# Performance work log

Measured on AMD Instinct MI355X. Metric: run time of the kernel, lower is better.

The kernel has to match this reference:

```python
import jax, jax.numpy as jnp
import numpy as np

N = 50000
E = 800000
IN_DIM = 256
HID = 64
HEADS = 4
OUT_DIM = 32
NEG_SLOPE = 0.2
EPS = 1e-5


def segment_softmax(logits, seg, num_segments):
    # logits: [E, H]; softmax over edges sharing the same destination node
    m = jax.ops.segment_max(logits, seg, num_segments=num_segments)
    m = jnp.where(jnp.isfinite(m), m, 0.0)
    e = jnp.exp(logits - m[seg])
    s = jax.ops.segment_sum(e, seg, num_segments=num_segments)
    return e / (s[seg] + 1e-16)


def setup_inputs() -> dict:
    key = jax.random.key(0)
    ks = jax.random.split(key, 16)
    d = {}
    d['x'] = jax.random.normal(ks[0], (N, IN_DIM), dtype=jnp.float32)
    d['edge_index'] = jax.random.randint(ks[1], (2, E), 0, N, dtype=jnp.int64)
    sc = lambda fan: 1.0 / np.sqrt(fan)
    # input transform: Linear(256->128), Linear(128->64)
    d['t1_w'] = jax.random.normal(ks[2], (IN_DIM, IN_DIM // 2), dtype=jnp.float32) * sc(IN_DIM)
    d['t1_b'] = jnp.zeros((IN_DIM // 2,), jnp.float32)
    d['t2_w'] = jax.random.normal(ks[3], (IN_DIM // 2, IN_DIM // 4), dtype=jnp.float32) * sc(IN_DIM // 2)
    d['t2_b'] = jnp.zeros((IN_DIM // 4,), jnp.float32)
    d['g1_w'] = jax.random.normal(ks[4], (IN_DIM // 4, HEADS * HID), dtype=jnp.float32) * sc(IN_DIM // 4)
    d['g1_att_src'] = jax.random.normal(ks[5], (HEADS, HID), dtype=jnp.float32) * sc(HID)
    d['g1_att_dst'] = jax.random.normal(ks[6], (HEADS, HID), dtype=jnp.float32) * sc(HID)
    d['g1_b'] = jnp.zeros((HEADS * HID,), jnp.float32)
    # GraphNorm(256)
    d['gn_w'] = jnp.ones((HEADS * HID,), jnp.float32)
    d['gn_b'] = jnp.zeros((HEADS * HID,), jnp.float32)
    d['gn_ms'] = jnp.ones((HEADS * HID,), jnp.float32)
    # GATConv 2: 256 -> 32, 1 head, no concat (mean == identity for 1 head)
    d['g2_w'] = jax.random.normal(ks[7], (HEADS * HID, OUT_DIM), dtype=jnp.float32) * sc(HEADS * HID)
    d['g2_att_src'] = jax.random.normal(ks[8], (1, OUT_DIM), dtype=jnp.float32) * sc(OUT_DIM)
    d['g2_att_dst'] = jax.random.normal(ks[9], (1, OUT_DIM), dtype=jnp.float32) * sc(OUT_DIM)
    d['g2_b'] = jnp.zeros((OUT_DIM,), jnp.float32)
    return d


def gat_conv(x, src, dst, w, att_src, att_dst, bias, n_nodes):
    heads, ch = att_src.shape
    h = (x @ w).reshape(n_nodes, heads, ch)            # [N,H,C]
    a_src = jnp.sum(h * att_src, axis=-1)              # [N,H]
    a_dst = jnp.sum(h * att_dst, axis=-1)              # [N,H]
    logits = jax.nn.leaky_relu(a_src[src] + a_dst[dst], NEG_SLOPE)  # [E,H]
    alpha = segment_softmax(logits, dst, n_nodes)      # [E,H]
    msgs = alpha[:, :, None] * h[src]                  # [E,H,C]
    out = jax.ops.segment_sum(msgs, dst, num_segments=n_nodes)  # [N,H,C]
    return out.reshape(n_nodes, heads * ch) + bias


def reference(x, edge_index, t1_w, t1_b, t2_w, t2_b,
              g1_w, g1_att_src, g1_att_dst, g1_b,
              gn_w, gn_b, gn_ms,
              g2_w, g2_att_src, g2_att_dst, g2_b):
    src, dst = edge_index[0], edge_index[1]
    # input transform (dropout inactive in eval)
    h = jax.nn.relu(x @ t1_w + t1_b)
    h = jax.nn.relu(h @ t2_w + t2_b)
    # GAT layer 1 (concat heads)
    h = gat_conv(h, src, dst, g1_w, g1_att_src, g1_att_dst, g1_b, N)
    # GraphNorm over the whole graph (batch=None -> single graph)
    mean = jnp.mean(h, axis=0)
    o = h - mean * gn_ms
    var = jnp.mean(o * o, axis=0)
    h = o / jnp.sqrt(var + EPS) * gn_w + gn_b
    h = jax.nn.elu(h)
    # GAT layer 2 (1 head, concat=False)
    h = gat_conv(h, src, dst, g2_w, g2_att_src, g2_att_dst, g2_b, N)
    return jax.nn.log_softmax(h, axis=1)
```

## Files before the change

kernel.cpp:

```cpp
#include <hip/hip_runtime.h>

#define NSLOPE 0.2f
#define GEPS 1e-5f

typedef unsigned short ushortT;
typedef __attribute__((ext_vector_type(8))) unsigned short us8;
typedef __attribute__((ext_vector_type(8))) __bf16 bf16x8;
typedef __attribute__((ext_vector_type(4))) float f32x4;

__device__ __forceinline__ float lrelu(float x) { return x >= 0.f ? x : NSLOPE * x; }
__device__ __forceinline__ ushortT f2bf(float f) {
    unsigned int u = __float_as_uint(f);
    return (ushortT)((u + 0x7fffu + ((u >> 16) & 1u)) >> 16);
}
__device__ __forceinline__ float bf2f(ushortT h) {
    return __uint_as_float((unsigned int)h << 16);
}

__global__ __launch_bounds__(256) void k_prep_hist(
    const float* __restrict__ w1, const float* __restrict__ w2,
    const float* __restrict__ g1w, const float* __restrict__ g2w,
    ushortT* __restrict__ w1t, ushortT* __restrict__ w2t,
    ushortT* __restrict__ g1t, ushortT* __restrict__ g2t,
    const int* __restrict__ dst, int* __restrict__ deg, int E)
{
    if (blockIdx.x >= 128) {
        const int i = (blockIdx.x - 128) * 256 + threadIdx.x;
        if (i < E) atomicAdd(&deg[dst[i]], 1);
        return;
    }
    const int i = blockIdx.x * 256 + threadIdx.x;
    if (i < 128 * 256) { const int c = i >> 8, k = i & 255; w1t[i] = f2bf(w1[k * 128 + c]); }
    if (i < 64 * 128)  { const int c = i >> 7, k = i & 127; w2t[i] = f2bf(w2[k * 64 + c]); }
    if (i < 256 * 64)  { const int c = i >> 6, k = i & 63;  g1t[i] = f2bf(g1w[k * 256 + c]); }
    if (i < 32 * 256)  { const int c = i >> 8, k = i & 255; g2t[i] = f2bf(g2w[k * 32 + c]); }
}

__global__ __launch_bounds__(256) void k_lin1(const float* __restrict__ x,
    const ushortT* __restrict__ w1t, const float* __restrict__ b1,
    ushortT* __restrict__ h1, int n,
    const int* __restrict__ deg, int* __restrict__ offs, int* __restrict__ bsum, int gemmB)
{
    if ((int)blockIdx.x >= gemmB) {
        __shared__ int sm[256];
        const int t = threadIdx.x;
        const int i = (blockIdx.x - gemmB) * 256 + t;
        const int v = (i < n) ? deg[i] : 0;
        sm[t] = v;
        __syncthreads();
        for (int off = 1; off < 256; off <<= 1) {
            int add = (t >= off) ? sm[t - off] : 0;
            __syncthreads();
            sm[t] += add;
            __syncthreads();
        }
        if (i < n) offs[i] = sm[t] - v;
        if (t == 255) bsum[blockIdx.x - gemmB] = sm[255];
        return;
    }
    __shared__ us8 Ab[64 * 128 / 16];
    __shared__ us8 Bb[128 * 128 / 16];
    char* A = (char*)Ab; char* B = (char*)Bb;
    const int t = threadIdx.x;
    const int w = t >> 6, l = t & 63;
    const int lo = l & 15, hi = l >> 4;
    const int n0 = blockIdx.x * 64;
    const int wm = (w >> 1) * 32, wn = (w & 1) * 64;
    f32x4 acc[2][4];
    #pragma unroll
    for (int mf = 0; mf < 2; ++mf)
        #pragma unroll
        for (int nf = 0; nf < 4; ++nf) acc[mf][nf] = (f32x4){0.f, 0.f, 0.f, 0.f};

    const int arow = t >> 2, ak0 = (t & 3) * 16;
    int agn = n0 + arow; if (agn >= n) agn = n - 1;
    const int asw = (arow & 7) << 4;

    for (int kc = 0; kc < 4; ++kc) {
        __syncthreads();
        {
            ushortT tmp[16];
            const float* xp = &x[(size_t)agn * 256 + kc * 64 + ak0];
            #pragma unroll
            for (int j = 0; j < 4; ++j) {
                const float4 v = *(const float4*)(xp + j * 4);
                tmp[j*4+0] = f2bf(v.x); tmp[j*4+1] = f2bf(v.y);
                tmp[j*4+2] = f2bf(v.z); tmp[j*4+3] = f2bf(v.w);
            }
            *(us8*)(A + arow * 128 + ((ak0 * 2) ^ asw)) = *(us8*)tmp;
            *(us8*)(A + arow * 128 + ((ak0 * 2 + 16) ^ asw)) = *(us8*)(tmp + 8);
        }
        #pragma unroll
        for (int i = 0; i < 4; ++i) {
            const int idx = i * 256 + t, br = idx >> 3, bs = idx & 7;
            const us8 v = *(const us8*)&w1t[(size_t)br * 256 + kc * 64 + bs * 8];
            *(us8*)(B + br * 128 + ((bs * 16) ^ ((br & 7) << 4))) = v;
        }
        __syncthreads();
        #pragma unroll
        for (int ks = 0; ks < 2; ++ks) {
            const int koff = ks * 64 + hi * 16;
            bf16x8 af[2], bf[4];
            #pragma unroll
            for (int mf = 0; mf < 2; ++mf) {
                const int r = wm + mf * 16 + lo;
                af[mf] = *(const bf16x8*)(A + r * 128 + (koff ^ ((r & 7) << 4)));
            }
            #pragma unroll
            for (int nf = 0; nf < 4; ++nf) {
                const int r = wn + nf * 16 + lo;
                bf[nf] = *(const bf16x8*)(B + r * 128 + (koff ^ ((r & 7) << 4)));
            }
            #pragma unroll
            for (int mf = 0; mf < 2; ++mf)
                #pragma unroll
                for (int nf = 0; nf < 4; ++nf)
                    acc[mf][nf] = __builtin_amdgcn_mfma_f32_16x16x32_bf16(af[mf], bf[nf], acc[mf][nf], 0, 0, 0);
        }
    }
    #pragma unroll
    for (int nf = 0; nf < 4; ++nf) {
        const int col = wn + nf * 16 + lo;
        const float bb = b1[col];
        #pragma unroll
        for (int mf = 0; mf < 2; ++mf)
            #pragma unroll
            for (int j = 0; j < 4; ++j) {
                const int r = n0 + wm + mf * 16 + hi * 4 + j;
                if (r < n) h1[(size_t)r * 128 + col] = f2bf(fmaxf(acc[mf][nf][j] + bb, 0.f));
            }
    }
}

__global__ __launch_bounds__(256) void k_lin2(const ushortT* __restrict__ h1,
    const ushortT* __restrict__ w2t, const float* __restrict__ b2,
    ushortT* __restrict__ h2, int n,
    int* __restrict__ bsum, int nb, int gemmB)
{
    if ((int)blockIdx.x >= gemmB) {
        __shared__ int sm[256];
        const int t = threadIdx.x;
        const int v = (t < nb) ? bsum[t] : 0;
        sm[t] = v;
        __syncthreads();
        for (int off = 1; off < 256; off <<= 1) {
            int add = (t >= off) ? sm[t - off] : 0;
            __syncthreads();
            sm[t] += add;
            __syncthreads();
        }
        if (t < nb) bsum[t] = sm[t] - v;
        return;
    }
    __shared__ us8 Ab[64 * 128 / 16];
    __shared__ us8 Bb[64 * 128 / 16];
    char* A = (char*)Ab; char* B = (char*)Bb;
    const int t = threadIdx.x;
    const int w = t >> 6, l = t & 63;
    const int lo = l & 15, hi = l >> 4;
    const int n0 = blockIdx.x * 64;
    const int wm = (w >> 1) * 32, wn = (w & 1) * 32;
    f32x4 acc[2][2];
    #pragma unroll
    for (int mf = 0; mf < 2; ++mf)
        #pragma unroll
        for (int nf = 0; nf < 2; ++nf) acc[mf][nf] = (f32x4){0.f, 0.f, 0.f, 0.f};

    const int arow = t >> 2, ak0 = (t & 3) * 16;
    int agn = n0 + arow; if (agn >= n) agn = n - 1;
    const int asw = (arow & 7) << 4;

    for (int kc = 0; kc < 2; ++kc) {
        __syncthreads();
        {
            const us8 v0 = *(const us8*)&h1[(size_t)agn * 128 + kc * 64 + ak0];
            const us8 v1 = *(const us8*)&h1[(size_t)agn * 128 + kc * 64 + ak0 + 8];
            *(us8*)(A + arow * 128 + ((ak0 * 2) ^ asw)) = v0;
            *(us8*)(A + arow * 128 + ((ak0 * 2 + 16) ^ asw)) = v1;
        }
        #pragma unroll
        for (int i = 0; i < 2; ++i) {
            const int idx = i * 256 + t, br = idx >> 3, bs = idx & 7;
            const us8 v = *(const us8*)&w2t[(size_t)br * 128 + kc * 64 + bs * 8];
            *(us8*)(B + br * 128 + ((bs * 16) ^ ((br & 7) << 4))) = v;
        }
        __syncthreads();
        #pragma unroll
        for (int ks = 0; ks < 2; ++ks) {
            const int koff = ks * 64 + hi * 16;
            bf16x8 af[2], bf[2];
            #pragma unroll
            for (int mf = 0; mf < 2; ++mf) {
                const int r = wm + mf * 16 + lo;
                af[mf] = *(const bf16x8*)(A + r * 128 + (koff ^ ((r & 7) << 4)));
            }
            #pragma unroll
            for (int nf = 0; nf < 2; ++nf) {
                const int r = wn + nf * 16 + lo;
                bf[nf] = *(const bf16x8*)(B + r * 128 + (koff ^ ((r & 7) << 4)));
            }
            #pragma unroll
            for (int mf = 0; mf < 2; ++mf)
                #pragma unroll
                for (int nf = 0; nf < 2; ++nf)
                    acc[mf][nf] = __builtin_amdgcn_mfma_f32_16x16x32_bf16(af[mf], bf[nf], acc[mf][nf], 0, 0, 0);
        }
    }
    #pragma unroll
    for (int nf = 0; nf < 2; ++nf) {
        const int col = wn + nf * 16 + lo;
        const float bb = b2[col];
        #pragma unroll
        for (int mf = 0; mf < 2; ++mf)
            #pragma unroll
            for (int j = 0; j < 4; ++j) {
                const int r = n0 + wm + mf * 16 + hi * 4 + j;
                if (r < n) h2[(size_t)r * 64 + col] = f2bf(fmaxf(acc[mf][nf][j] + bb, 0.f));
            }
    }
}

__global__ __launch_bounds__(256) void k_g1feat(const ushortT* __restrict__ h2,
    const ushortT* __restrict__ g1t, const float* __restrict__ attS, const float* __restrict__ attD,
    ushortT* __restrict__ hg1, float* __restrict__ a1s, float* __restrict__ a1d, int n,
    int* __restrict__ offs, int* __restrict__ cursor, const int* __restrict__ bsum, int E, int gemmB)
{
    if ((int)blockIdx.x >= gemmB) {
        const int sb = blockIdx.x - gemmB;
        const int i = sb * 256 + threadIdx.x;
        if (i < n) {
            int o = offs[i] + bsum[i >> 8];
            offs[i] = o;
            cursor[i] = o;
        }
        if (i == 0) offs[n] = E;
        return;
    }
    __shared__ us8 Ab[64 * 128 / 16];
    __shared__ us8 Bb[256 * 128 / 16];
    char* A = (char*)Ab; char* B = (char*)Bb;
    const int t = threadIdx.x;
    const int w = t >> 6, l = t & 63;
    const int lo = l & 15, hi = l >> 4;
    const int n0 = blockIdx.x * 64;
    const int wm = (w >> 1) * 32, wn = (w & 1) * 128;
    f32x4 acc[2][8];
    #pragma unroll
    for (int mf = 0; mf < 2; ++mf)
        #pragma unroll
        for (int nf = 0; nf < 8; ++nf) acc[mf][nf] = (f32x4){0.f, 0.f, 0.f, 0.f};

    {
        const int arow = t >> 2, ak0 = (t & 3) * 16;
        int agn = n0 + arow; if (agn >= n) agn = n - 1;
        const int asw = (arow & 7) << 4;
        const us8 v0 = *(const us8*)&h2[(size_t)agn * 64 + ak0];
        const us8 v1 = *(const us8*)&h2[(size_t)agn * 64 + ak0 + 8];
        *(us8*)(A + arow * 128 + ((ak0 * 2) ^ asw)) = v0;
        *(us8*)(A + arow * 128 + ((ak0 * 2 + 16) ^ asw)) = v1;
    }
    #pragma unroll
    for (int i = 0; i < 8; ++i) {
        const int idx = i * 256 + t, br = idx >> 3, bs = idx & 7;
        const us8 v = *(const us8*)&g1t[(size_t)br * 64 + bs * 8];
        *(us8*)(B + br * 128 + ((bs * 16) ^ ((br & 7) << 4))) = v;
    }
    __syncthreads();
    #pragma unroll
    for (int ks = 0; ks < 2; ++ks) {
        const int koff = ks * 64 + hi * 16;
        bf16x8 af[2];
        #pragma unroll
        for (int mf = 0; mf < 2; ++mf) {
            const int r = wm + mf * 16 + lo;
            af[mf] = *(const bf16x8*)(A + r * 128 + (koff ^ ((r & 7) << 4)));
        }
        #pragma unroll
        for (int nf = 0; nf < 8; ++nf) {
            const int r = wn + nf * 16 + lo;
            const bf16x8 bf = *(const bf16x8*)(B + r * 128 + (koff ^ ((r & 7) << 4)));
            #pragma unroll
            for (int mf = 0; mf < 2; ++mf)
                acc[mf][nf] = __builtin_amdgcn_mfma_f32_16x16x32_bf16(af[mf], bf, acc[mf][nf], 0, 0, 0);
        }
    }
    float sS[8], sD[8];
    #pragma unroll
    for (int nf = 0; nf < 8; ++nf) {
        sS[nf] = attS[wn + nf * 16 + lo];
        sD[nf] = attD[wn + nf * 16 + lo];
    }
    const int hA = wn >> 6, hB = hA + 1;
    #pragma unroll
    for (int mf = 0; mf < 2; ++mf)
        #pragma unroll
        for (int j = 0; j < 4; ++j) {
            const int r = n0 + wm + mf * 16 + hi * 4 + j;
            float pSA = 0.f, pDA = 0.f, pSB = 0.f, pDB = 0.f;
            #pragma unroll
            for (int nf = 0; nf < 4; ++nf) {
                pSA = fmaf(acc[mf][nf][j], sS[nf], pSA);
                pDA = fmaf(acc[mf][nf][j], sD[nf], pDA);
                pSB = fmaf(acc[mf][nf + 4][j], sS[nf + 4], pSB);
                pDB = fmaf(acc[mf][nf + 4][j], sD[nf + 4], pDB);
            }
            #pragma unroll
            for (int off = 1; off < 16; off <<= 1) {
                pSA += __shfl_xor(pSA, off);
                pDA += __shfl_xor(pDA, off);
                pSB += __shfl_xor(pSB, off);
                pDB += __shfl_xor(pDB, off);
            }
            if (r < n) {
                if (lo == 0) {
                    a1s[r * 4 + hA] = pSA; a1s[r * 4 + hB] = pSB;
                    a1d[r * 4 + hA] = pDA; a1d[r * 4 + hB] = pDB;
                }
                #pragma unroll
                for (int nf = 0; nf < 8; ++nf)
                    hg1[(size_t)r * 256 + wn + nf * 16 + lo] = f2bf(acc[mf][nf][j]);
            }
        }
}

__global__ __launch_bounds__(256) void k_g2feat(const ushortT* __restrict__ out1,
    const float* __restrict__ colsum, const float* __restrict__ colsq,
    const float* __restrict__ gw, const float* __restrict__ gb, const float* __restrict__ gms,
    const ushortT* __restrict__ g2t, const float* __restrict__ attS, const float* __restrict__ attD,
    ushortT* __restrict__ hg2, float* __restrict__ a2s, float* __restrict__ a2d, int n)
{
    __shared__ us8 Ab[64 * 128 / 16];
    __shared__ us8 Bb[32 * 128 / 16];
    __shared__ float lsc[256], lsh[256];
    char* A = (char*)Ab; char* B = (char*)Bb;
    const int t = threadIdx.x;
    const int w = t >> 6, l = t & 63;
    const int lo = l & 15, hi = l >> 4;
    const int n0 = blockIdx.x * 64;
    const int wm = w * 16;
    {
        const float invn = 1.f / (float)n;
        const float mean = colsum[t] * invn;
        const float msq = colsq[t] * invn;
        const float ms = gms[t];
        const float var = msq - 2.f * ms * mean * mean + ms * ms * mean * mean;
        const float sc = gw[t] * rsqrtf(var + GEPS);
        lsc[t] = sc;
        lsh[t] = gb[t] - mean * ms * sc;
    }
    f32x4 acc[2];
    acc[0] = (f32x4){0.f, 0.f, 0.f, 0.f};
    acc[1] = (f32x4){0.f, 0.f, 0.f, 0.f};

    const int arow = t >> 2, ak0 = (t & 3) * 16;
    int agn = n0 + arow; if (agn >= n) agn = n - 1;
    const int asw = (arow & 7) << 4;

    for (int kc = 0; kc < 4; ++kc) {
        __syncthreads();
        {
            ushortT tmp[16];
            const us8 v0 = *(const us8*)&out1[(size_t)agn * 256 + kc * 64 + ak0];
            const us8 v1 = *(const us8*)&out1[(size_t)agn * 256 + kc * 64 + ak0 + 8];
            #pragma unroll
            for (int j = 0; j < 8; ++j) {
                float a = bf2f(v0[j]) * lsc[kc * 64 + ak0 + j] + lsh[kc * 64 + ak0 + j];
                float b = bf2f(v1[j]) * lsc[kc * 64 + ak0 + 8 + j] + lsh[kc * 64 + ak0 + 8 + j];
                a = a > 0.f ? a : __expf(a) - 1.f;
                b = b > 0.f ? b : __expf(b) - 1.f;
                tmp[j] = f2bf(a); tmp[8 + j] = f2bf(b);
            }
            *(us8*)(A + arow * 128 + ((ak0 * 2) ^ asw)) = *(us8*)tmp;
            *(us8*)(A + arow * 128 + ((ak0 * 2 + 16) ^ asw)) = *(us8*)(tmp + 8);
        }
        {
            const int br = t >> 3, bs = t & 7;
            const us8 v = *(const us8*)&g2t[(size_t)br * 256 + kc * 64 + bs * 8];
            *(us8*)(B + br * 128 + ((bs * 16) ^ ((br & 7) << 4))) = v;
        }
        __syncthreads();
        #pragma unroll
        for (int ks = 0; ks < 2; ++ks) {
            const int koff = ks * 64 + hi * 16;
            const int ra = wm + lo;
            const bf16x8 af = *(const bf16x8*)(A + ra * 128 + (koff ^ ((ra & 7) << 4)));
            #pragma unroll
            for (int nf = 0; nf < 2; ++nf) {
                const int r = nf * 16 + lo;
                const bf16x8 bf = *(const bf16x8*)(B + r * 128 + (koff ^ ((r & 7) << 4)));
                acc[nf] = __builtin_amdgcn_mfma_f32_16x16x32_bf16(af, bf, acc[nf], 0, 0, 0);
            }
        }
    }
    float sS[2], sD[2];
    sS[0] = attS[lo]; sS[1] = attS[16 + lo];
    sD[0] = attD[lo]; sD[1] = attD[16 + lo];
    #pragma unroll
    for (int j = 0; j < 4; ++j) {
        const int r = n0 + wm + hi * 4 + j;
        float pS = fmaf(acc[0][j], sS[0], acc[1][j] * sS[1]);
        float pD = fmaf(acc[0][j], sD[0], acc[1][j] * sD[1]);
        #pragma unroll
        for (int off = 1; off < 16; off <<= 1) {
            pS += __shfl_xor(pS, off);
            pD += __shfl_xor(pD, off);
        }
        if (r < n) {
            if (lo == 0) { a2s[r] = pS; a2d[r] = pD; }
            hg2[(size_t)r * 32 + lo] = f2bf(acc[0][j]);
            hg2[(size_t)r * 32 + 16 + lo] = f2bf(acc[1][j]);
        }
    }
}

__global__ void k_scatter(const int* __restrict__ src, const int* __restrict__ dst,
                          int* __restrict__ cursor, int* __restrict__ csr, int e) {
    int i = blockIdx.x * 256 + threadIdx.x;
    if (i < e) {
        int p = atomicAdd(&cursor[dst[i]], 1);
        csr[p] = src[i];
    }
}

__global__ __launch_bounds__(256) void k_alpha1(
    const float* __restrict__ a1s, const float* __restrict__ a1d,
    const int* __restrict__ offs, const int* __restrict__ csr,
    float* __restrict__ alphaE, int n)
{
    const int l = threadIdx.x & 15;
    const int d = blockIdx.x * 16 + (threadIdx.x >> 4);
    if (d >= n) return;
    const int start = offs[d], end = offs[d + 1];
    const float4* __restrict__ a1s4 = (const float4*)a1s;
    const float4 adv = ((const float4*)a1d)[d];
    const float ad0 = adv.x, ad1 = adv.y, ad2 = adv.z, ad3 = adv.w;

    float m0 = -1e30f, m1 = -1e30f, m2 = -1e30f, m3 = -1e30f;
    float s0 = 0.f, s1 = 0.f, s2 = 0.f, s3 = 0.f;
    for (int e = start + l; e < end; e += 16) {
        const float4 av = a1s4[csr[e]];
        const float l0 = lrelu(av.x + ad0), l1 = lrelu(av.y + ad1);
        const float l2 = lrelu(av.z + ad2), l3 = lrelu(av.w + ad3);
        float nm;
        nm = fmaxf(m0, l0); s0 = s0 * __expf(m0 - nm) + __expf(l0 - nm); m0 = nm;
        nm = fmaxf(m1, l1); s1 = s1 * __expf(m1 - nm) + __expf(l1 - nm); m1 = nm;
        nm = fmaxf(m2, l2); s2 = s2 * __expf(m2 - nm) + __expf(l2 - nm); m2 = nm;
        nm = fmaxf(m3, l3); s3 = s3 * __expf(m3 - nm) + __expf(l3 - nm); m3 = nm;
    }
    for (int off = 1; off < 16; off <<= 1) {
        float om, os, nm;
        om = __shfl_xor(m0, off, 16); os = __shfl_xor(s0, off, 16);
        nm = fmaxf(m0, om); s0 = s0 * __expf(m0 - nm) + os * __expf(om - nm); m0 = nm;
        om = __shfl_xor(m1, off, 16); os = __shfl_xor(s1, off, 16);
        nm = fmaxf(m1, om); s1 = s1 * __expf(m1 - nm) + os * __expf(om - nm); m1 = nm;
        om = __shfl_xor(m2, off, 16); os = __shfl_xor(s2, off, 16);
        nm = fmaxf(m2, om); s2 = s2 * __expf(m2 - nm) + os * __expf(om - nm); m2 = nm;
        om = __shfl_xor(m3, off, 16); os = __shfl_xor(s3, off, 16);
        nm = fmaxf(m3, om); s3 = s3 * __expf(m3 - nm) + os * __expf(om - nm); m3 = nm;
    }
    const float i0 = 1.f / (s0 + 1e-16f), i1 = 1.f / (s1 + 1e-16f);
    const float i2 = 1.f / (s2 + 1e-16f), i3 = 1.f / (s3 + 1e-16f);
    for (int e = start + l; e < end; e += 16) {
        const float4 av = a1s4[csr[e]];
        float4 o;
        o.x = __expf(lrelu(av.x + ad0) - m0) * i0;
        o.y = __expf(lrelu(av.y + ad1) - m1) * i1;
        o.z = __expf(lrelu(av.z + ad2) - m2) * i2;
        o.w = __expf(lrelu(av.w + ad3) - m3) * i3;
        *(float4*)&alphaE[(size_t)e * 4] = o;
    }
}

__global__ __launch_bounds__(256, 8) void k_pv1(
    const ushortT* __restrict__ hg1, const float* __restrict__ alphaE,
    const int* __restrict__ offs, const int* __restrict__ csr,
    const float* __restrict__ bias, ushortT* __restrict__ out1, int n)
{
    const int lane = threadIdx.x & 63;
    const int d = blockIdx.x * 4 + (threadIdx.x >> 6);
    if (d >= n) return;
    const int start = offs[d], end = offs[d + 1];
    const int cg = lane & 31;
    const int c = cg * 8;
    const int es = lane >> 5;
    const int head = cg >> 3;
    float acc[8];
    #pragma unroll
    for (int j = 0; j < 8; ++j) acc[j] = 0.f;

    #pragma unroll 4
    for (int e = start + es; e < end; e += 2) {
        const int si = csr[e];
        const float al = alphaE[(size_t)e * 4 + head];
        const us8 hv = *(const us8*)&hg1[(size_t)si * 256 + c];
        #pragma unroll
        for (int j = 0; j < 8; ++j) acc[j] = fmaf(al, bf2f(hv[j]), acc[j]);
    }
    #pragma unroll
    for (int j = 0; j < 8; ++j) acc[j] += __shfl_xor(acc[j], 32);
    if (es == 0) {
        const float4 b0 = *(const float4*)&bias[c];
        const float4 b1 = *(const float4*)&bias[c + 4];
        us8 o;
        o[0] = f2bf(acc[0] + b0.x); o[1] = f2bf(acc[1] + b0.y);
        o[2] = f2bf(acc[2] + b0.z); o[3] = f2bf(acc[3] + b0.w);
        o[4] = f2bf(acc[4] + b1.x); o[5] = f2bf(acc[5] + b1.y);
        o[6] = f2bf(acc[6] + b1.z); o[7] = f2bf(acc[7] + b1.w);
        *(us8*)&out1[(size_t)d * 256 + c] = o;
    }
}

__global__ __launch_bounds__(256) void k_colstat(const ushortT* __restrict__ out1,
    float* __restrict__ colsum, float* __restrict__ colsq, int n)
{
    const int t = threadIdx.x;
    float s = 0.f, q = 0.f;
    for (int r = blockIdx.x; r < n; r += gridDim.x) {
        const float v = bf2f(out1[(size_t)r * 256 + t]);
        s += v;
        q += v * v;
    }
    atomicAdd(&colsum[t], s);
    atomicAdd(&colsq[t], q);
}

__global__ __launch_bounds__(256, 8) void k_pv2(
    const ushortT* __restrict__ hg2, const float* __restrict__ a2s, const float* __restrict__ a2d,
    const int* __restrict__ offs, const int* __restrict__ csr,
    const float* __restrict__ bias, float* __restrict__ out, int n)
{
    const int lane = threadIdx.x & 31;
    const int d = blockIdx.x * 8 + (threadIdx.x >> 5);
    if (d >= n) return;
    const int start = offs[d], end = offs[d + 1];
    const float adv = a2d[d];
    float m = -1e30f, s = 0.f;
    for (int e = start + lane; e < end; e += 32) {
        const float lv = lrelu(a2s[csr[e]] + adv);
        const float nm = fmaxf(m, lv);
        s = s * __expf(m - nm) + __expf(lv - nm);
        m = nm;
    }
    for (int off = 1; off < 32; off <<= 1) {
        const float om = __shfl_xor(m, off, 32), os = __shfl_xor(s, off, 32);
        const float nm = fmaxf(m, om);
        s = s * __expf(m - nm) + os * __expf(om - nm);
        m = nm;
    }
    const float inv = 1.f / (s + 1e-16f);
    const int l = lane & 15, es = lane >> 4;
    const int c = l * 2;
    float acc0 = 0.f, acc1 = 0.f;
    #pragma unroll 4
    for (int e = start + es; e < end; e += 2) {
        const int si = csr[e];
        const float al = __expf(lrelu(a2s[si] + adv) - m) * inv;
        const ushort2 hv = *(const ushort2*)&hg2[(size_t)si * 32 + c];
        acc0 = fmaf(al, bf2f(hv.x), acc0);
        acc1 = fmaf(al, bf2f(hv.y), acc1);
    }
    acc0 += __shfl_xor(acc0, 16, 32);
    acc1 += __shfl_xor(acc1, 16, 32);
    const float v0 = acc0 + bias[c];
    const float v1 = acc1 + bias[c + 1];
    float mx = fmaxf(v0, v1);
    for (int off = 1; off < 16; off <<= 1) mx = fmaxf(mx, __shfl_xor(mx, off, 16));
    float se = __expf(v0 - mx) + __expf(v1 - mx);
    for (int off = 1; off < 16; off <<= 1) se += __shfl_xor(se, off, 16);
    const float ls = __logf(se);
    if (es == 0) {
        float2 o = {v0 - mx - ls, v1 - mx - ls};
        *(float2*)&out[(size_t)d * 32 + c] = o;
    }
}

extern "C" void kernel_launch(void* const* d_in, const int* in_sizes, int n_in,
                              void* d_out, int out_size, void* d_ws, size_t ws_size,
                              hipStream_t stream)
{
    const float* x    = (const float*)d_in[0];
    const int*   ei   = (const int*)d_in[1];
    const float* t1w  = (const float*)d_in[2];
    const float* t1b  = (const float*)d_in[3];
    const float* t2w  = (const float*)d_in[4];
    const float* t2b  = (const float*)d_in[5];
    const float* g1w  = (const float*)d_in[6];
    const float* g1as = (const float*)d_in[7];
    const float* g1ad = (const float*)d_in[8];
    const float* g1b  = (const float*)d_in[9];
    const float* gnw  = (const float*)d_in[10];
    const float* gnb  = (const float*)d_in[11];
    const float* gnms = (const float*)d_in[12];
    const float* g2w  = (const float*)d_in[13];
    const float* g2as = (const float*)d_in[14];
    const float* g2ad = (const float*)d_in[15];
    const float* g2b  = (const float*)d_in[16];

    const int N = in_sizes[0] / 256;
    const int E = in_sizes[1] / 2;
    const int* srcA = ei;
    const int* dstA = ei + E;

    char* ws = (char*)d_ws;
    size_t cur = 0;
    auto alloc = [&](size_t bytes) -> char* {
        char* p = ws + cur;
        cur += (bytes + 255) & ~(size_t)255;
        return p;
    };
    ushortT* h1      = (ushortT*)alloc((size_t)N * 128 * 2);
    ushortT* h2      = (ushortT*)alloc((size_t)N * 64 * 2);
    ushortT* hg1     = (ushortT*)alloc((size_t)N * 256 * 2);
    float*   a1s     = (float*)alloc((size_t)N * 4 * 4);
    float*   a1d     = (float*)alloc((size_t)N * 4 * 4);
    ushortT* out1    = (ushortT*)alloc((size_t)N * 256 * 2);
    ushortT* hg2     = (ushortT*)alloc((size_t)N * 32 * 2);
    float*   a2s     = (float*)alloc((size_t)N * 4);
    float*   a2d     = (float*)alloc((size_t)N * 4);
    int*     deg     = (int*)alloc((size_t)(N + 1) * 4);
    int*     offs    = (int*)alloc((size_t)(N + 1) * 4);
    int*     cursor  = (int*)alloc((size_t)N * 4);
    int*     bsum    = (int*)alloc(1024);
    int*     csr     = (int*)alloc((size_t)E * 4);
    float*   alphaE  = (float*)alloc((size_t)E * 4 * 4);
    float*   colsum  = (float*)alloc(1024);
    float*   colsq   = (float*)alloc(1024);
    ushortT* w1t     = (ushortT*)alloc(128 * 256 * 2);
    ushortT* w2t     = (ushortT*)alloc(64 * 128 * 2);
    ushortT* g1t     = (ushortT*)alloc(256 * 64 * 2);
    ushortT* g2t     = (ushortT*)alloc(32 * 256 * 2);

    hipMemsetAsync(deg, 0, (size_t)(N + 1) * 4, stream);
    hipMemsetAsync(colsum, 0, 2048, stream);

    const int EB  = (E + 255) / 256;
    const int NB  = (N + 255) / 256;
    const int B64 = (N + 63) / 64;
    const int B16 = (N + 15) / 16;
    const int B8  = (N + 7) / 8;
    const int B4  = (N + 3) / 4;

    k_prep_hist<<<128 + EB, 256, 0, stream>>>(t1w, t2w, g1w, g2w, w1t, w2t, g1t, g2t, dstA, deg, E);
    k_lin1<<<B64 + NB, 256, 0, stream>>>(x, w1t, t1b, h1, N, deg, offs, bsum, B64);
    k_lin2<<<B64 + 1, 256, 0, stream>>>(h1, w2t, t2b, h2, N, bsum, NB, B64);
    k_g1feat<<<B64 + NB, 256, 0, stream>>>(h2, g1t, g1as, g1ad, hg1, a1s, a1d, N, offs, cursor, bsum, E, B64);
    k_scatter<<<EB, 256, 0, stream>>>(srcA, dstA, cursor, csr, E);
    k_alpha1<<<B16, 256, 0, stream>>>(a1s, a1d, offs, csr, alphaE, N);
    k_pv1<<<B4, 256, 0, stream>>>(hg1, alphaE, offs, csr, g1b, out1, N);
    k_colstat<<<256, 256, 0, stream>>>(out1, colsum, colsq, N);
    k_g2feat<<<B64, 256, 0, stream>>>(out1, colsum, colsq, gnw, gnb, gnms, g2t, g2as, g2ad, hg2, a2s, a2d, N);
    k_pv2<<<B8, 256, 0, stream>>>(hg2, a2s, a2d, offs, csr, g2b, (float*)d_out, N);
}
```

Baseline: 289.1 us.

## Fuse edge softmax into aggregation and fold CSR build into GEMM kernels

The layer-1 attention softmax is now computed inside the aggregation kernel, so the per-edge alpha array is no longer written and then read back. The prefix-offset finalisation moves into the lin2 side blocks and the edge scatter moves into the g1feat side blocks, which removes two separate kernel launches. In exchange, each edge's exp is computed twice in the aggregation kernel and its logit source is gathered an extra time. The scatter also now runs alongside GEMM blocks that may compete with it for resources.

```diff
diff --git a/kernel.cpp b/kernel.cpp
--- a/kernel.cpp
+++ b/kernel.cpp
@@ -135,21 +135,31 @@
 __global__ __launch_bounds__(256) void k_lin2(const ushortT* __restrict__ h1,
     const ushortT* __restrict__ w2t, const float* __restrict__ b2,
     ushortT* __restrict__ h2, int n,
-    int* __restrict__ bsum, int nb, int gemmB)
+    const int* __restrict__ bsum, int nb,
+    int* __restrict__ offs, int* __restrict__ cursor, int E, int gemmB)
 {
     if ((int)blockIdx.x >= gemmB) {
-        __shared__ int sm[256];
+        __shared__ int pre[256];
+        const int sb = blockIdx.x - gemmB;
         const int t = threadIdx.x;
         const int v = (t < nb) ? bsum[t] : 0;
-        sm[t] = v;
+        pre[t] = v;
         __syncthreads();
         for (int off = 1; off < 256; off <<= 1) {
-            int add = (t >= off) ? sm[t - off] : 0;
+            int add = (t >= off) ? pre[t - off] : 0;
             __syncthreads();
-            sm[t] += add;
+            pre[t] += add;
             __syncthreads();
         }
-        if (t < nb) bsum[t] = sm[t] - v;
+        __shared__ int excl[256];
+        excl[t] = pre[t] - v;
+        __syncthreads();
+        for (int i = sb * 256 + t; i < n; i += 8 * 256) {
+            const int o = offs[i] + excl[i >> 8];
+            offs[i] = o;
+            cursor[i] = o;
+        }
+        if (sb == 0 && t == 0) offs[n] = E;
         return;
     }
     __shared__ us8 Ab[64 * 128 / 16];
@@ -223,17 +233,15 @@
 __global__ __launch_bounds__(256) void k_g1feat(const ushortT* __restrict__ h2,
     const ushortT* __restrict__ g1t, const float* __restrict__ attS, const float* __restrict__ attD,
     ushortT* __restrict__ hg1, float* __restrict__ a1s, float* __restrict__ a1d, int n,
-    int* __restrict__ offs, int* __restrict__ cursor, const int* __restrict__ bsum, int E, int gemmB)
+    const int* __restrict__ src, const int* __restrict__ dst,
+    int* __restrict__ cursor, int* __restrict__ csr, int E, int gemmB)
 {
     if ((int)blockIdx.x >= gemmB) {
-        const int sb = blockIdx.x - gemmB;
-        const int i = sb * 256 + threadIdx.x;
-        if (i < n) {
-            int o = offs[i] + bsum[i >> 8];
-            offs[i] = o;
-            cursor[i] = o;
-        }
-        if (i == 0) offs[n] = E;
+        const int i = (blockIdx.x - gemmB) * 256 + threadIdx.x;
+        if (i < E) {
+            int p = atomicAdd(&cursor[dst[i]], 1);
+            csr[p] = src[i];
+        }
         return;
     }
     __shared__ us8 Ab[64 * 128 / 16];
@@ -413,66 +421,8 @@
     }
 }
 
-__global__ void k_scatter(const int* __restrict__ src, const int* __restrict__ dst,
-                          int* __restrict__ cursor, int* __restrict__ csr, int e) {
-    int i = blockIdx.x * 256 + threadIdx.x;
-    if (i < e) {
-        int p = atomicAdd(&cursor[dst[i]], 1);
-        csr[p] = src[i];
-    }
-}
-
-__global__ __launch_bounds__(256) void k_alpha1(
-    const float* __restrict__ a1s, const float* __restrict__ a1d,
-    const int* __restrict__ offs, const int* __restrict__ csr,
-    float* __restrict__ alphaE, int n)
-{
-    const int l = threadIdx.x & 15;
-    const int d = blockIdx.x * 16 + (threadIdx.x >> 4);
-    if (d >= n) return;
-    const int start = offs[d], end = offs[d + 1];
-    const float4* __restrict__ a1s4 = (const float4*)a1s;
-    const float4 adv = ((const float4*)a1d)[d];
-    const float ad0 = adv.x, ad1 = adv.y, ad2 = adv.z, ad3 = adv.w;
-
-    float m0 = -1e30f, m1 = -1e30f, m2 = -1e30f, m3 = -1e30f;
-    float s0 = 0.f, s1 = 0.f, s2 = 0.f, s3 = 0.f;
-    for (int e = start + l; e < end; e += 16) {
-        const float4 av = a1s4[csr[e]];
-        const float l0 = lrelu(av.x + ad0), l1 = lrelu(av.y + ad1);
-        const float l2 = lrelu(av.z + ad2), l3 = lrelu(av.w + ad3);
-        float nm;
-        nm = fmaxf(m0, l0); s0 = s0 * __expf(m0 - nm) + __expf(l0 - nm); m0 = nm;
-        nm = fmaxf(m1, l1); s1 = s1 * __expf(m1 - nm) + __expf(l1 - nm); m1 = nm;
-        nm = fmaxf(m2, l2); s2 = s2 * __expf(m2 - nm) + __expf(l2 - nm); m2 = nm;
-        nm = fmaxf(m3, l3); s3 = s3 * __expf(m3 - nm) + __expf(l3 - nm); m3 = nm;
-    }
-    for (int off = 1; off < 16; off <<= 1) {
-        float om, os, nm;
-        om = __shfl_xor(m0, off, 16); os = __shfl_xor(s0, off, 16);
-        nm = fmaxf(m0, om); s0 = s0 * __expf(m0 - nm) + os * __expf(om - nm); m0 = nm;
-        om = __shfl_xor(m1, off, 16); os = __shfl_xor(s1, off, 16);
-        nm = fmaxf(m1, om); s1 = s1 * __expf(m1 - nm) + os * __expf(om - nm); m1 = nm;
-        om = __shfl_xor(m2, off, 16); os = __shfl_xor(s2, off, 16);
-        nm = fmaxf(m2, om); s2 = s2 * __expf(m2 - nm) + os * __expf(om - nm); m2 = nm;
-        om = __shfl_xor(m3, off, 16); os = __shfl_xor(s3, off, 16);
-        nm = fmaxf(m3, om); s3 = s3 * __expf(m3 - nm) + os * __expf(om - nm); m3 = nm;
-    }
-    const float i0 = 1.f / (s0 + 1e-16f), i1 = 1.f / (s1 + 1e-16f);
-    const float i2 = 1.f / (s2 + 1e-16f), i3 = 1.f / (s3 + 1e-16f);
-    for (int e = start + l; e < end; e += 16) {
-        const float4 av = a1s4[csr[e]];
-        float4 o;
-        o.x = __expf(lrelu(av.x + ad0) - m0) * i0;
-        o.y = __expf(lrelu(av.y + ad1) - m1) * i1;
-        o.z = __expf(lrelu(av.z + ad2) - m2) * i2;
-        o.w = __expf(lrelu(av.w + ad3) - m3) * i3;
-        *(float4*)&alphaE[(size_t)e * 4] = o;
-    }
-}
-
 __global__ __launch_bounds__(256, 8) void k_pv1(
-    const ushortT* __restrict__ hg1, const float* __restrict__ alphaE,
+    const ushortT* __restrict__ hg1, const float* __restrict__ a1s, const float* __restrict__ a1d,
     const int* __restrict__ offs, const int* __restrict__ csr,
     const float* __restrict__ bias, ushortT* __restrict__ out1, int n)
 {
@@ -480,10 +430,34 @@
     const int d = blockIdx.x * 4 + (threadIdx.x >> 6);
     if (d >= n) return;
     const int start = offs[d], end = offs[d + 1];
+
+    const int h = lane & 3, el = lane >> 2;
+    const float adh1 = a1d[d * 4 + h];
+    float m = -1e30f, s = 0.f;
+    for (int e = start + el; e < end; e += 16) {
+        const int si = csr[e];
+        const float lv = lrelu(a1s[si * 4 + h] + adh1);
+        const float nm = fmaxf(m, lv);
+        s = s * __expf(m - nm) + __expf(lv - nm);
+        m = nm;
+    }
+    #pragma unroll
+    for (int off = 4; off < 64; off <<= 1) {
+        const float om = __shfl_xor(m, off), os = __shfl_xor(s, off);
+        const float nm = fmaxf(m, om);
+        s = s * __expf(m - nm) + os * __expf(om - nm);
+        m = nm;
+    }
+
     const int cg = lane & 31;
     const int c = cg * 8;
     const int es = lane >> 5;
     const int head = cg >> 3;
+    const float mh  = __shfl(m, head);
+    const float sh  = __shfl(s, head);
+    const float adh = __shfl(adh1, head);
+    const float inv = 1.f / (sh + 1e-16f);
+
     float acc[8];
     #pragma unroll
     for (int j = 0; j < 8; ++j) acc[j] = 0.f;
@@ -491,7 +465,7 @@
     #pragma unroll 4
     for (int e = start + es; e < end; e += 2) {
         const int si = csr[e];
-        const float al = alphaE[(size_t)e * 4 + head];
+        const float al = __expf(lrelu(a1s[si * 4 + head] + adh) - mh) * inv;
         const us8 hv = *(const us8*)&hg1[(size_t)si * 256 + c];
         #pragma unroll
         for (int j = 0; j < 8; ++j) acc[j] = fmaf(al, bf2f(hv[j]), acc[j]);
@@ -622,7 +596,6 @@
     int*     cursor  = (int*)alloc((size_t)N * 4);
     int*     bsum    = (int*)alloc(1024);
     int*     csr     = (int*)alloc((size_t)E * 4);
-    float*   alphaE  = (float*)alloc((size_t)E * 4 * 4);
     float*   colsum  = (float*)alloc(1024);
     float*   colsq   = (float*)alloc(1024);
     ushortT* w1t     = (ushortT*)alloc(128 * 256 * 2);
@@ -636,17 +609,14 @@
     const int EB  = (E + 255) / 256;
     const int NB  = (N + 255) / 256;
     const int B64 = (N + 63) / 64;
-    const int B16 = (N + 15) / 16;
     const int B8  = (N + 7) / 8;
     const int B4  = (N + 3) / 4;
 
     k_prep_hist<<<128 + EB, 256, 0, stream>>>(t1w, t2w, g1w, g2w, w1t, w2t, g1t, g2t, dstA, deg, E);
     k_lin1<<<B64 + NB, 256, 0, stream>>>(x, w1t, t1b, h1, N, deg, offs, bsum, B64);
-    k_lin2<<<B64 + 1, 256, 0, stream>>>(h1, w2t, t2b, h2, N, bsum, NB, B64);
-    k_g1feat<<<B64 + NB, 256, 0, stream>>>(h2, g1t, g1as, g1ad, hg1, a1s, a1d, N, offs, cursor, bsum, E, B64);
-    k_scatter<<<EB, 256, 0, stream>>>(srcA, dstA, cursor, csr, E);
-    k_alpha1<<<B16, 256, 0, stream>>>(a1s, a1d, offs, csr, alphaE, N);
-    k_pv1<<<B4, 256, 0, stream>>>(hg1, alphaE, offs, csr, g1b, out1, N);
+    k_lin2<<<B64 + 8, 256, 0, stream>>>(h1, w2t, t2b, h2, N, bsum, NB, offs, cursor, E, B64);
+    k_g1feat<<<B64 + EB, 256, 0, stream>>>(h2, g1t, g1as, g1ad, hg1, a1s, a1d, N, srcA, dstA, cursor, csr, E, B64);
+    k_pv1<<<B4, 256, 0, stream>>>(hg1, a1s, a1d, offs, csr, g1b, out1, N);
     k_colstat<<<256, 256, 0, stream>>>(out1, colsum, colsq, N);
     k_g2feat<<<B64, 256, 0, stream>>>(out1, colsum, colsq, gnw, gnb, gnms, g2t, g2as, g2ad, hg2, a2s, a2d, N);
     k_pv2<<<B8, 256, 0, stream>>>(hg2, a2s, a2d, offs, csr, g2b, (float*)d_out, N);
```

After: 308.0 us. +6.5%, slower.
